# Kernel tuning notes

Measured on AMD Instinct MI355X. Metric: run time of the kernel, lower is better.

The kernel has to match this reference:

```python
import jax, jax.numpy as jnp
import numpy as np

G = 16          # horizontal stripes
K = 4           # latents per stripe
TEMP = 0.125
TOPK_RATIO = 0.125
GATE_THR = 0.05
EPS = 1e-6
KSZ = 3


def setup_inputs() -> dict:
    key = jax.random.key(0)
    k1, k2 = jax.random.split(key)
    x = jax.random.normal(k1, (64, 256, 64, 44), dtype=jnp.float32)
    latent_basis = jax.random.normal(k2, (G, K, 256), dtype=jnp.float32)
    return {"x": x, "latent_basis": latent_basis}


def _avg_pool3(x):
    # x: [n, g, c, sh, w]; 3x3 avg pool, stride 1, pad 1, count_include_pad=True
    s = jax.lax.reduce_window(x, 0.0, jax.lax.add,
                              (1, 1, 1, KSZ, KSZ), (1, 1, 1, 1, 1),
                              [(0, 0), (0, 0), (0, 0), (1, 1), (1, 1)])
    return s / float(KSZ * KSZ)


def _l2norm(v, axis=-1):
    return v / jnp.maximum(jnp.linalg.norm(v, axis=axis, keepdims=True), 1e-12)


def reference(x, latent_basis):
    n, c, h, w = x.shape
    sh = h // G
    p = sh * w
    # split into horizontal stripes: [n, g, c, sh, w]
    xr = x.reshape(n, c, G, sh, w).transpose(0, 2, 1, 3, 4)
    support_feat = _avg_pool3(xr)
    feat_flat = xr.transpose(0, 1, 3, 4, 2).reshape(n, G, p, c)          # ngpc
    support_flat = support_feat.transpose(0, 1, 3, 4, 2).reshape(n, G, p, c)

    # active mask from detached feature energy
    e = jax.lax.stop_gradient(xr).astype(jnp.float32)
    fe = jnp.mean(e * e, axis=2)                                          # n g sh w
    fe = fe / jnp.maximum(jnp.max(fe, axis=(-2, -1), keepdims=True), EPS)
    active = (fe > GATE_THR).astype(jnp.float32)
    fallback = (fe > 0).astype(jnp.float32)
    use_fb = jnp.sum(active, axis=(-2, -1), keepdims=True) <= 0
    active = jnp.where(use_fb, fallback, active).reshape(n, G, p)

    # cosine-similarity routing
    sfn = _l2norm(support_flat)
    lbn = _l2norm(latent_basis)                                           # g k c
    logits = jnp.einsum('ngpc,gkc->ngpk', sfn, lbn) / TEMP
    route_prob = jax.nn.softmax(logits, axis=-1)
    support = route_prob * active[..., None]                              # n g p k
    pool_w = support / jnp.maximum(jnp.sum(support, axis=2, keepdims=True), EPS)
    tokens = jnp.einsum('ngpk,ngpc->ngkc', pool_w, feat_flat)
    tokens = tokens.transpose(0, 3, 1, 2).reshape(n, c, G * K)            # n c (g k)

    # top-k presence
    kk = max(1, min(p, int(p * TOPK_RATIO)))
    topv, _ = jax.lax.top_k(support.transpose(0, 1, 3, 2), kk)            # n g k kk
    presence = jnp.mean(topv, axis=-1).reshape(n, G * K)
    presence = presence / jnp.maximum(jnp.sum(presence, axis=1, keepdims=True), EPS)

    # scatter per-stripe maps back into full-resolution zero tensors
    eye = jnp.eye(G, dtype=support.dtype)
    loc_s = support.reshape(n, G, sh, w, K).transpose(0, 1, 4, 2, 3)      # n g k sh w
    loc_p = pool_w.reshape(n, G, sh, w, K).transpose(0, 1, 4, 2, 3)
    smap = jnp.einsum('ngksw,gG->ngkGsw', loc_s, eye).reshape(n, G * K, h, w)
    pmap = jnp.einsum('ngksw,gG->ngkGsw', loc_p, eye).reshape(n, G * K, h, w)
    support_flat_global = smap.transpose(0, 2, 3, 1).reshape(n, h * w, G * K)
    pool_weights_flat_global = pmap.transpose(0, 2, 3, 1).reshape(n, h * w, G * K)

    return (tokens.astype(x.dtype), presence.astype(x.dtype),
            support_flat_global.astype(x.dtype), pool_weights_flat_global.astype(x.dtype))
```

## Files before the change

### kernel.cpp

```cpp
#include <hip/hip_runtime.h>
#include <math.h>

#define GG   16
#define KK   4
#define NN   64
#define CC   256
#define SHH  4
#define WW   44
#define PP   176
#define HWSZ 2816
#define CHW  720896
#define TOPKK 22

template<int CTRL, int RMASK>
__device__ __forceinline__ float dpp0(float v) {
    return __int_as_float(__builtin_amdgcn_update_dpp(
        0, __float_as_int(v), CTRL, RMASK, 0xF, true));
}

__device__ __forceinline__ float wave_sum63(float v) {
    v += dpp0<0x111, 0xF>(v);
    v += dpp0<0x112, 0xF>(v);
    v += dpp0<0x114, 0xF>(v);
    v += dpp0<0x118, 0xF>(v);
    v += dpp0<0x142, 0xA>(v);
    v += dpp0<0x143, 0xC>(v);
    return v;
}
__device__ __forceinline__ float bcast63(float v) {
    return __int_as_float(__builtin_amdgcn_readlane(__float_as_int(v), 63));
}
__device__ __forceinline__ float wave_sum_all(float v) { return bcast63(wave_sum63(v)); }

__device__ __forceinline__ float wave_max_nn(float v) {
    v = fmaxf(v, dpp0<0x111, 0xF>(v));
    v = fmaxf(v, dpp0<0x112, 0xF>(v));
    v = fmaxf(v, dpp0<0x114, 0xF>(v));
    v = fmaxf(v, dpp0<0x118, 0xF>(v));
    v = fmaxf(v, dpp0<0x142, 0xA>(v));
    v = fmaxf(v, dpp0<0x143, 0xC>(v));
    return bcast63(v);
}

__global__ __launch_bounds__(64) void norm_basis_kernel(
    const float* __restrict__ lb, float* __restrict__ lbn) {
    const int gk = blockIdx.x;
    const int lane = threadIdx.x;
    const float* row = lb + (size_t)gk * CC;
    float v0 = row[lane], v1 = row[lane + 64], v2 = row[lane + 128], v3 = row[lane + 192];
    float ss = v0 * v0 + v1 * v1 + v2 * v2 + v3 * v3;
    float tot = wave_sum_all(ss);
    float sc = 1.0f / fmaxf(sqrtf(tot), 1e-12f);
    const int g = gk >> 2, k = gk & 3;
    float* dst = lbn + (size_t)g * CC * 4 + k;
    dst[(size_t)lane * 4]        = v0 * sc;
    dst[(size_t)(lane + 64) * 4]  = v1 * sc;
    dst[(size_t)(lane + 128) * 4] = v2 * sc;
    dst[(size_t)(lane + 192) * 4] = v3 * sc;
}

__global__ __launch_bounds__(256) void stripe_kernel(
    const float* __restrict__ x, const float* __restrict__ lbn,
    float* __restrict__ sup_ws, float* __restrict__ pw_ws,
    float* __restrict__ pres_ws, float* __restrict__ tok_out) {
    const int g = blockIdx.x;
    const int n = blockIdx.y;
    const int tid = threadIdx.x;
    const int s = tid >> 6;
    const int lane = tid & 63;
    const bool al = lane < WW;

    __shared__ float4 Xq[2][SHH][WW];
    __shared__ float4 Hq[2][SHH][WW];
    __shared__ float4 sup4[PP];
    __shared__ float4 pw4[PP];
    __shared__ float redA[SHH];
    __shared__ float redB[SHH];
    __shared__ float zred[SHH][4];

    const size_t nbase = (size_t)n * CHW + (size_t)g * PP;
    const float* xrow = x + nbase + s * WW + (al ? lane : 0);
    const float4* lbg = (const float4*)lbn + (g << 8);

    float d0 = 0, d1 = 0, d2 = 0, d3 = 0, nrm = 0, fe = 0;

    int buf = 0;
    float4 xv, Hv;
    for (int c0 = 0; c0 < CC; c0 += 4, buf ^= 1) {
        if (al) {
            xv.x = xrow[(size_t)(c0 + 0) * HWSZ];
            xv.y = xrow[(size_t)(c0 + 1) * HWSZ];
            xv.z = xrow[(size_t)(c0 + 2) * HWSZ];
            xv.w = xrow[(size_t)(c0 + 3) * HWSZ];
            fe += xv.x * xv.x + xv.y * xv.y + xv.z * xv.z + xv.w * xv.w;
            Xq[buf][s][lane] = xv;
        }
        __syncthreads();
        if (al) {
            float4 L = {0, 0, 0, 0}, R = {0, 0, 0, 0};
            if (lane > 0)      L = Xq[buf][s][lane - 1];
            if (lane < WW - 1) R = Xq[buf][s][lane + 1];
            Hv.x = xv.x + L.x + R.x;
            Hv.y = xv.y + L.y + R.y;
            Hv.z = xv.z + L.z + R.z;
            Hv.w = xv.w + L.w + R.w;
            Hq[buf][s][lane] = Hv;
        }
        __syncthreads();
        if (al) {
            float4 U = {0, 0, 0, 0}, D = {0, 0, 0, 0};
            if (s > 0)       U = Hq[buf][s - 1][lane];
            if (s < SHH - 1) D = Hq[buf][s + 1][lane];
            const float k9 = 1.0f / 9.0f;
            float p0 = (Hv.x + U.x + D.x) * k9;
            float p1 = (Hv.y + U.y + D.y) * k9;
            float p2 = (Hv.z + U.z + D.z) * k9;
            float p3 = (Hv.w + U.w + D.w) * k9;
            nrm += p0 * p0 + p1 * p1 + p2 * p2 + p3 * p3;
            float4 l0 = lbg[c0], l1 = lbg[c0 + 1], l2 = lbg[c0 + 2], l3 = lbg[c0 + 3];
            d0 += p0 * l0.x + p1 * l1.x + p2 * l2.x + p3 * l3.x;
            d1 += p0 * l0.y + p1 * l1.y + p2 * l2.y + p3 * l3.y;
            d2 += p0 * l0.z + p1 * l1.z + p2 * l2.z + p3 * l3.z;
            d3 += p0 * l0.w + p1 * l1.w + p2 * l2.w + p3 * l3.w;
        }
    }

    fe *= (1.0f / 256.0f);
    float fmw = wave_max_nn(al ? fe : 0.0f);
    if (lane == 0) redA[s] = fmw;
    __syncthreads();
    float femax = fmaxf(fmaxf(redA[0], redA[1]), fmaxf(redA[2], redA[3]));
    float den = fmaxf(femax, 1e-6f);
    bool pa = al && ((fe / den) > 0.05f);
    unsigned long long bl = __ballot((int)pa);
    if (lane == 0) redB[s] = (float)__popcll(bl);
    __syncthreads();
    float cnt = redB[0] + redB[1] + redB[2] + redB[3];
    float actv = pa ? 1.0f : 0.0f;
    if (cnt <= 0.0f) actv = (al && (fe > 0.0f)) ? 1.0f : 0.0f;

    float inv = 8.0f / fmaxf(sqrtf(nrm), 1e-12f);
    float L0 = d0 * inv, L1 = d1 * inv, L2 = d2 * inv, L3 = d3 * inv;
    float mx = fmaxf(fmaxf(L0, L1), fmaxf(L2, L3));
    float e0 = expf(L0 - mx), e1 = expf(L1 - mx), e2 = expf(L2 - mx), e3 = expf(L3 - mx);
    float esum = e0 + e1 + e2 + e3;
    float sc = actv / esum;
    float s0 = e0 * sc, s1 = e1 * sc, s2 = e2 * sc, s3 = e3 * sc;

    float z0 = wave_sum63(s0), z1 = wave_sum63(s1), z2 = wave_sum63(s2), z3 = wave_sum63(s3);
    if (lane == 63) { zred[s][0] = z0; zred[s][1] = z1; zred[s][2] = z2; zred[s][3] = z3; }
    __syncthreads();
    float Z0 = zred[0][0] + zred[1][0] + zred[2][0] + zred[3][0];
    float Z1 = zred[0][1] + zred[1][1] + zred[2][1] + zred[3][1];
    float Z2 = zred[0][2] + zred[1][2] + zred[2][2] + zred[3][2];
    float Z3 = zred[0][3] + zred[1][3] + zred[2][3] + zred[3][3];
    float q0 = s0 / fmaxf(Z0, 1e-6f);
    float q1 = s1 / fmaxf(Z1, 1e-6f);
    float q2 = s2 / fmaxf(Z2, 1e-6f);
    float q3 = s3 / fmaxf(Z3, 1e-6f);

    if (al) {
        const int p = s * WW + lane;
        float4 sv = make_float4(s0, s1, s2, s3);
        float4 qv = make_float4(q0, q1, q2, q3);
        sup4[p] = sv;
        pw4[p] = qv;
        const size_t wsb = ((size_t)(n * GG + g) * PP + p);
        ((float4*)sup_ws)[wsb] = sv;
        ((float4*)pw_ws)[wsb] = qv;
    }
    __syncthreads();

    {
        const float* supf = (const float*)sup4;
        const int k = s;
        float v0 = supf[lane * 4 + k];
        float v1 = supf[(lane + 64) * 4 + k];
        float v2 = (lane < PP - 128) ? supf[(lane + 128) * 4 + k] : -1e30f;
        float tks = 0.0f;
        for (int it = 0; it < TOPKK; ++it) {
            float lm = fmaxf(v0, fmaxf(v1, v2));
            float M = wave_max_nn(lm);
            tks += M;
            unsigned long long mk = __ballot((int)(lm == M));
            int src = __ffsll(mk) - 1;
            if (lane == src) {
                if (v0 == M)      v0 = -1e30f;
                else if (v1 == M) v1 = -1e30f;
                else              v2 = -1e30f;
            }
        }
        if (lane == 0) pres_ws[(size_t)n * 64 + g * KK + k] = tks * (1.0f / (float)TOPKK);
    }

    float4 pwa = pw4[lane];
    float4 pwb = pw4[lane + 64];
    float4 pwc = (lane < PP - 128) ? pw4[lane + 128] : make_float4(0, 0, 0, 0);
    const float* xb2 = x + nbase;
    float* tokg = tok_out + (size_t)n * CC * 64 + g * KK;
    for (int i = 0; i < 64; ++i) {
        const int c = (s << 6) + i;
        const float* xc = xb2 + (size_t)c * HWSZ;
        float a0 = xc[lane];
        float a1 = xc[lane + 64];
        float a2 = (lane < PP - 128) ? xc[lane + 128] : 0.0f;
        float t0 = a0 * pwa.x + a1 * pwb.x + a2 * pwc.x;
        float t1 = a0 * pwa.y + a1 * pwb.y + a2 * pwc.y;
        float t2 = a0 * pwa.z + a1 * pwb.z + a2 * pwc.z;
        float t3 = a0 * pwa.w + a1 * pwb.w + a2 * pwc.w;
        t0 = wave_sum63(t0); t1 = wave_sum63(t1); t2 = wave_sum63(t2); t3 = wave_sum63(t3);
        if (lane == 63) {
            *(float4*)(tokg + (size_t)c * 64) = make_float4(t0, t1, t2, t3);
        }
    }
}

__global__ __launch_bounds__(256) void scatter_kernel(
    const float* __restrict__ sup_ws, const float* __restrict__ pw_ws,
    float* __restrict__ outS, float* __restrict__ outP) {
    const int t = blockIdx.x * 256 + threadIdx.x;
    const int g = t & 15;
    const int rest = t >> 4;
    const int yx = rest % HWSZ;
    const int n = rest / HWSZ;
    const int y = yx / WW;
    const int xx = yx - y * WW;
    float4 vs = make_float4(0, 0, 0, 0);
    float4 vp = make_float4(0, 0, 0, 0);
    if (g == (y >> 2)) {
        const int p = (y & 3) * WW + xx;
        const size_t base = ((size_t)(n * GG + g) * PP + p);
        vs = ((const float4*)sup_ws)[base];
        vp = ((const float4*)pw_ws)[base];
    }
    ((float4*)outS)[t] = vs;
    ((float4*)outP)[t] = vp;
}

__global__ __launch_bounds__(64) void presence_kernel(
    const float* __restrict__ pres_ws, float* __restrict__ outp) {
    const int n = blockIdx.x;
    const int lane = threadIdx.x;
    float v = pres_ws[(size_t)n * 64 + lane];
    float tot = wave_sum_all(v);
    outp[(size_t)n * 64 + lane] = v / fmaxf(tot, 1e-6f);
}

extern "C" void kernel_launch(void* const* d_in, const int* in_sizes, int n_in,
                              void* d_out, int out_size, void* d_ws, size_t ws_size,
                              hipStream_t stream) {
    const float* x = (const float*)d_in[0];
    const float* lb = (const float*)d_in[1];
    float* ws = (float*)d_ws;
    float* lbn    = ws;
    float* sup_ws = lbn + 16384;
    float* pw_ws  = sup_ws + 720896;
    float* pres_ws = pw_ws + 720896;

    float* out = (float*)d_out;
    float* tok   = out;
    float* pres  = out + 1048576;
    float* outS  = out + 1052672;
    float* outP  = outS + 11534336;

    norm_basis_kernel<<<GG * KK, 64, 0, stream>>>(lb, lbn);
    stripe_kernel<<<dim3(GG, NN), 256, 0, stream>>>(x, lbn, sup_ws, pw_ws, pres_ws, tok);
    scatter_kernel<<<(NN * HWSZ * 16) / 256, 256, 0, stream>>>(sup_ws, pw_ws, outS, outP);
    presence_kernel<<<NN, 64, 0, stream>>>(pres_ws, pres);
}
```

Before: 351.1 us.

## Split stripe kernel into channel-chunked partial, finalize and token kernels

```diff
diff --git a/kernel.cpp b/kernel.cpp
--- a/kernel.cpp
+++ b/kernel.cpp
@@ -11,6 +11,8 @@
 #define HWSZ 2816
 #define CHW  720896
 #define TOPKK 22
+#define NCHUNK 2
+#define CPC  128
 
 template<int CTRL, int RMASK>
 __device__ __forceinline__ float dpp0(float v) {
@@ -53,17 +55,17 @@
     float sc = 1.0f / fmaxf(sqrtf(tot), 1e-12f);
     const int g = gk >> 2, k = gk & 3;
     float* dst = lbn + (size_t)g * CC * 4 + k;
-    dst[(size_t)lane * 4]        = v0 * sc;
+    dst[(size_t)lane * 4]         = v0 * sc;
     dst[(size_t)(lane + 64) * 4]  = v1 * sc;
     dst[(size_t)(lane + 128) * 4] = v2 * sc;
     dst[(size_t)(lane + 192) * 4] = v3 * sc;
 }
 
-__global__ __launch_bounds__(256) void stripe_kernel(
+__global__ __launch_bounds__(256) void part_kernel(
     const float* __restrict__ x, const float* __restrict__ lbn,
-    float* __restrict__ sup_ws, float* __restrict__ pw_ws,
-    float* __restrict__ pres_ws, float* __restrict__ tok_out) {
-    const int g = blockIdx.x;
+    float4* __restrict__ dpart, float2* __restrict__ nfpart) {
+    const int g = blockIdx.x & 15;
+    const int chunk = blockIdx.x >> 4;
     const int n = blockIdx.y;
     const int tid = threadIdx.x;
     const int s = tid >> 6;
@@ -72,21 +74,17 @@
 
     __shared__ float4 Xq[2][SHH][WW];
     __shared__ float4 Hq[2][SHH][WW];
-    __shared__ float4 sup4[PP];
-    __shared__ float4 pw4[PP];
-    __shared__ float redA[SHH];
-    __shared__ float redB[SHH];
-    __shared__ float zred[SHH][4];
 
     const size_t nbase = (size_t)n * CHW + (size_t)g * PP;
     const float* xrow = x + nbase + s * WW + (al ? lane : 0);
     const float4* lbg = (const float4*)lbn + (g << 8);
+    const int cbase = chunk * CPC;
 
     float d0 = 0, d1 = 0, d2 = 0, d3 = 0, nrm = 0, fe = 0;
 
     int buf = 0;
     float4 xv, Hv;
-    for (int c0 = 0; c0 < CC; c0 += 4, buf ^= 1) {
+    for (int c0 = cbase; c0 < cbase + CPC; c0 += 4, buf ^= 1) {
         if (al) {
             xv.x = xrow[(size_t)(c0 + 0) * HWSZ];
             xv.y = xrow[(size_t)(c0 + 1) * HWSZ];
@@ -124,6 +122,40 @@
             d3 += p0 * l0.w + p1 * l1.w + p2 * l2.w + p3 * l3.w;
         }
     }
+    if (al) {
+        const size_t idx = (((size_t)(n * GG + g) * NCHUNK) + chunk) * PP + s * WW + lane;
+        dpart[idx] = make_float4(d0, d1, d2, d3);
+        nfpart[idx] = make_float2(nrm, fe);
+    }
+}
+
+__global__ __launch_bounds__(256) void finalize_kernel(
+    const float4* __restrict__ dpart, const float2* __restrict__ nfpart,
+    float* __restrict__ sup_ws, float* __restrict__ pw_ws,
+    float* __restrict__ pres_ws) {
+    const int g = blockIdx.x;
+    const int n = blockIdx.y;
+    const int tid = threadIdx.x;
+    const int s = tid >> 6;
+    const int lane = tid & 63;
+    const bool al = lane < WW;
+
+    __shared__ float4 sup4[PP];
+    __shared__ float redA[SHH];
+    __shared__ float redB[SHH];
+    __shared__ float zred[SHH][4];
+
+    float d0 = 0, d1 = 0, d2 = 0, d3 = 0, nrm = 0, fe = 0;
+    if (al) {
+        const int p = s * WW + lane;
+        const size_t b = (size_t)(n * GG + g) * NCHUNK * PP + p;
+        for (int ch = 0; ch < NCHUNK; ++ch) {
+            float4 dv = dpart[b + ch * PP];
+            float2 nf = nfpart[b + ch * PP];
+            d0 += dv.x; d1 += dv.y; d2 += dv.z; d3 += dv.w;
+            nrm += nf.x; fe += nf.y;
+        }
+    }
 
     fe *= (1.0f / 256.0f);
     float fmw = wave_max_nn(al ? fe : 0.0f);
@@ -164,7 +196,6 @@
         float4 sv = make_float4(s0, s1, s2, s3);
         float4 qv = make_float4(q0, q1, q2, q3);
         sup4[p] = sv;
-        pw4[p] = qv;
         const size_t wsb = ((size_t)(n * GG + g) * PP + p);
         ((float4*)sup_ws)[wsb] = sv;
         ((float4*)pw_ws)[wsb] = qv;
@@ -192,15 +223,29 @@
         }
         if (lane == 0) pres_ws[(size_t)n * 64 + g * KK + k] = tks * (1.0f / (float)TOPKK);
     }
-
-    float4 pwa = pw4[lane];
-    float4 pwb = pw4[lane + 64];
-    float4 pwc = (lane < PP - 128) ? pw4[lane + 128] : make_float4(0, 0, 0, 0);
-    const float* xb2 = x + nbase;
+}
+
+__global__ __launch_bounds__(256) void token_kernel(
+    const float* __restrict__ x, const float* __restrict__ pw_ws,
+    float* __restrict__ tok_out) {
+    const int g = blockIdx.x & 15;
+    const int chunk = blockIdx.x >> 4;
+    const int n = blockIdx.y;
+    const int tid = threadIdx.x;
+    const int s = tid >> 6;
+    const int lane = tid & 63;
+
+    const float4* pwq = (const float4*)pw_ws + (size_t)(n * GG + g) * PP;
+    float4 pwa = pwq[lane];
+    float4 pwb = pwq[lane + 64];
+    float4 pwc = (lane < PP - 128) ? pwq[lane + 128] : make_float4(0, 0, 0, 0);
+
+    const float* xb = x + (size_t)n * CHW + (size_t)g * PP;
     float* tokg = tok_out + (size_t)n * CC * 64 + g * KK;
-    for (int i = 0; i < 64; ++i) {
-        const int c = (s << 6) + i;
-        const float* xc = xb2 + (size_t)c * HWSZ;
+    const int cb = chunk * CPC + s * (CPC / 4);
+    for (int i = 0; i < CPC / 4; ++i) {
+        const int c = cb + i;
+        const float* xc = xb + (size_t)c * HWSZ;
         float a0 = xc[lane];
         float a1 = xc[lane + 64];
         float a2 = (lane < PP - 128) ? xc[lane + 128] : 0.0f;
@@ -216,25 +261,33 @@
 }
 
 __global__ __launch_bounds__(256) void scatter_kernel(
-    const float* __restrict__ sup_ws, const float* __restrict__ pw_ws,
-    float* __restrict__ outS, float* __restrict__ outP) {
-    const int t = blockIdx.x * 256 + threadIdx.x;
-    const int g = t & 15;
-    const int rest = t >> 4;
-    const int yx = rest % HWSZ;
-    const int n = rest / HWSZ;
-    const int y = yx / WW;
-    const int xx = yx - y * WW;
-    float4 vs = make_float4(0, 0, 0, 0);
-    float4 vp = make_float4(0, 0, 0, 0);
-    if (g == (y >> 2)) {
+    const float4* __restrict__ sup_ws4, const float4* __restrict__ pw_ws4,
+    float4* __restrict__ outS, float4* __restrict__ outP) {
+    const int n = blockIdx.y;
+    const int pix0 = blockIdx.x * 16;
+    const int t = threadIdx.x;
+    __shared__ float4 qs[16];
+    __shared__ float4 qp[16];
+    if (t < 32) {
+        const int px = t & 15;
+        const int pixel = pix0 + px;
+        const int y = pixel / WW;
+        const int xx = pixel - y * WW;
+        const int g = y >> 2;
         const int p = (y & 3) * WW + xx;
-        const size_t base = ((size_t)(n * GG + g) * PP + p);
-        vs = ((const float4*)sup_ws)[base];
-        vp = ((const float4*)pw_ws)[base];
-    }
-    ((float4*)outS)[t] = vs;
-    ((float4*)outP)[t] = vp;
+        const size_t base = (size_t)(n * GG + g) * PP + p;
+        if (t < 16) qs[px] = sup_ws4[base];
+        else        qp[px] = pw_ws4[base];
+    }
+    __syncthreads();
+    const int px = t >> 4;
+    const int q = t & 15;
+    const int pixel = pix0 + px;
+    const int g = (pixel / WW) >> 2;
+    const float4 z = make_float4(0, 0, 0, 0);
+    const size_t o = ((size_t)n * HWSZ + pixel) * 16 + q;
+    outS[o] = (q == g) ? qs[px] : z;
+    outP[o] = (q == g) ? qp[px] : z;
 }
 
 __global__ __launch_bounds__(64) void presence_kernel(
@@ -252,19 +305,26 @@
     const float* x = (const float*)d_in[0];
     const float* lb = (const float*)d_in[1];
     float* ws = (float*)d_ws;
-    float* lbn    = ws;
-    float* sup_ws = lbn + 16384;
-    float* pw_ws  = sup_ws + 720896;
+    float* lbn     = ws;
+    float* sup_ws  = lbn + 16384;
+    float* pw_ws   = sup_ws + 720896;
     float* pres_ws = pw_ws + 720896;
 
     float* out = (float*)d_out;
-    float* tok   = out;
-    float* pres  = out + 1048576;
-    float* outS  = out + 1052672;
-    float* outP  = outS + 11534336;
+    float* tok  = out;
+    float* pres = out + 1048576;
+    float* outS = out + 1052672;
+    float* outP = outS + 11534336;
+
+    float4* dpart  = (float4*)outP;
+    float2* nfpart = (float2*)(outP + 1441792 * 4 / 1);
+    nfpart = (float2*)(outP + 5767168);
 
     norm_basis_kernel<<<GG * KK, 64, 0, stream>>>(lb, lbn);
-    stripe_kernel<<<dim3(GG, NN), 256, 0, stream>>>(x, lbn, sup_ws, pw_ws, pres_ws, tok);
-    scatter_kernel<<<(NN * HWSZ * 16) / 256, 256, 0, stream>>>(sup_ws, pw_ws, outS, outP);
+    part_kernel<<<dim3(GG * NCHUNK, NN), 256, 0, stream>>>(x, lbn, dpart, nfpart);
+    finalize_kernel<<<dim3(GG, NN), 256, 0, stream>>>(dpart, nfpart, sup_ws, pw_ws, pres_ws);
+    token_kernel<<<dim3(GG * NCHUNK, NN), 256, 0, stream>>>(x, pw_ws, tok);
+    scatter_kernel<<<dim3(HWSZ / 16, NN), 256, 0, stream>>>(
+        (const float4*)sup_ws, (const float4*)pw_ws, (float4*)outS, (float4*)outP);
     presence_kernel<<<NN, 64, 0, stream>>>(pres_ws, pres);
 }
```

Result: no change. 349.1 us (-0.6%).

## Fuse scatter into stripe kernel and split channel reduction across eight waves

Applied to the files above, without the earlier changes.

```diff
diff --git a/kernel.cpp b/kernel.cpp
--- a/kernel.cpp
+++ b/kernel.cpp
@@ -17,6 +17,8 @@
     return __int_as_float(__builtin_amdgcn_update_dpp(
         0, __float_as_int(v), CTRL, RMASK, 0xF, true));
 }
+__device__ __forceinline__ float nbrL(float v) { return dpp0<0x138, 0xF>(v); }
+__device__ __forceinline__ float nbrR(float v) { return dpp0<0x130, 0xF>(v); }
 
 __device__ __forceinline__ float wave_sum63(float v) {
     v += dpp0<0x111, 0xF>(v);
@@ -53,94 +55,119 @@
     float sc = 1.0f / fmaxf(sqrtf(tot), 1e-12f);
     const int g = gk >> 2, k = gk & 3;
     float* dst = lbn + (size_t)g * CC * 4 + k;
-    dst[(size_t)lane * 4]        = v0 * sc;
+    dst[(size_t)lane * 4]         = v0 * sc;
     dst[(size_t)(lane + 64) * 4]  = v1 * sc;
     dst[(size_t)(lane + 128) * 4] = v2 * sc;
     dst[(size_t)(lane + 192) * 4] = v3 * sc;
 }
 
-__global__ __launch_bounds__(256) void stripe_kernel(
+__global__ __launch_bounds__(512, 8) void fused_kernel(
     const float* __restrict__ x, const float* __restrict__ lbn,
-    float* __restrict__ sup_ws, float* __restrict__ pw_ws,
-    float* __restrict__ pres_ws, float* __restrict__ tok_out) {
+    float* __restrict__ pres_ws, float* __restrict__ tok_out,
+    float4* __restrict__ outS, float4* __restrict__ outP) {
     const int g = blockIdx.x;
     const int n = blockIdx.y;
     const int tid = threadIdx.x;
-    const int s = tid >> 6;
+    const int w = tid >> 6;
     const int lane = tid & 63;
     const bool al = lane < WW;
 
-    __shared__ float4 Xq[2][SHH][WW];
-    __shared__ float4 Hq[2][SHH][WW];
-    __shared__ float4 sup4[PP];
-    __shared__ float4 pw4[PP];
-    __shared__ float redA[SHH];
-    __shared__ float redB[SHH];
-    __shared__ float zred[SHH][4];
-
-    const size_t nbase = (size_t)n * CHW + (size_t)g * PP;
-    const float* xrow = x + nbase + s * WW + (al ? lane : 0);
+    __shared__ float4 pd[8][PP];
+    __shared__ float2 pnf[8][PP];
+    __shared__ float redA[4], redB[4], zred[4][4];
+    float4* sup4 = pd[2];
+    float4* pw4  = pd[4];
+
+    const float* xb = x + (size_t)n * CHW + g * PP;
     const float4* lbg = (const float4*)lbn + (g << 8);
 
-    float d0 = 0, d1 = 0, d2 = 0, d3 = 0, nrm = 0, fe = 0;
-
-    int buf = 0;
-    float4 xv, Hv;
-    for (int c0 = 0; c0 < CC; c0 += 4, buf ^= 1) {
-        if (al) {
-            xv.x = xrow[(size_t)(c0 + 0) * HWSZ];
-            xv.y = xrow[(size_t)(c0 + 1) * HWSZ];
-            xv.z = xrow[(size_t)(c0 + 2) * HWSZ];
-            xv.w = xrow[(size_t)(c0 + 3) * HWSZ];
-            fe += xv.x * xv.x + xv.y * xv.y + xv.z * xv.z + xv.w * xv.w;
-            Xq[buf][s][lane] = xv;
-        }
-        __syncthreads();
-        if (al) {
-            float4 L = {0, 0, 0, 0}, R = {0, 0, 0, 0};
-            if (lane > 0)      L = Xq[buf][s][lane - 1];
-            if (lane < WW - 1) R = Xq[buf][s][lane + 1];
-            Hv.x = xv.x + L.x + R.x;
-            Hv.y = xv.y + L.y + R.y;
-            Hv.z = xv.z + L.z + R.z;
-            Hv.w = xv.w + L.w + R.w;
-            Hq[buf][s][lane] = Hv;
-        }
-        __syncthreads();
-        if (al) {
-            float4 U = {0, 0, 0, 0}, D = {0, 0, 0, 0};
-            if (s > 0)       U = Hq[buf][s - 1][lane];
-            if (s < SHH - 1) D = Hq[buf][s + 1][lane];
-            const float k9 = 1.0f / 9.0f;
-            float p0 = (Hv.x + U.x + D.x) * k9;
-            float p1 = (Hv.y + U.y + D.y) * k9;
-            float p2 = (Hv.z + U.z + D.z) * k9;
-            float p3 = (Hv.w + U.w + D.w) * k9;
-            nrm += p0 * p0 + p1 * p1 + p2 * p2 + p3 * p3;
-            float4 l0 = lbg[c0], l1 = lbg[c0 + 1], l2 = lbg[c0 + 2], l3 = lbg[c0 + 3];
-            d0 += p0 * l0.x + p1 * l1.x + p2 * l2.x + p3 * l3.x;
-            d1 += p0 * l0.y + p1 * l1.y + p2 * l2.y + p3 * l3.y;
-            d2 += p0 * l0.z + p1 * l1.z + p2 * l2.z + p3 * l3.z;
-            d3 += p0 * l0.w + p1 * l1.w + p2 * l2.w + p3 * l3.w;
-        }
-    }
-
-    fe *= (1.0f / 256.0f);
-    float fmw = wave_max_nn(al ? fe : 0.0f);
-    if (lane == 0) redA[s] = fmw;
+    float4 dk[4];
+    float nr[4] = {0, 0, 0, 0}, fe[4] = {0, 0, 0, 0};
+    #pragma unroll
+    for (int s = 0; s < 4; ++s) dk[s] = make_float4(0, 0, 0, 0);
+
+    const int c0 = w * 32;
+    float r0 = 0, r1 = 0, r2 = 0, r3 = 0;
+    if (al) {
+        const float* xc = xb + (size_t)c0 * HWSZ;
+        r0 = xc[lane]; r1 = xc[lane + 44]; r2 = xc[lane + 88]; r3 = xc[lane + 132];
+    }
+    #pragma unroll 1
+    for (int i = 0; i < 32; ++i) {
+        float b0 = 0, b1 = 0, b2 = 0, b3 = 0;
+        if (i < 31 && al) {
+            const float* xn = xb + (size_t)(c0 + i + 1) * HWSZ;
+            b0 = xn[lane]; b1 = xn[lane + 44]; b2 = xn[lane + 88]; b3 = xn[lane + 132];
+        }
+        float4 lb = lbg[c0 + i];
+        fe[0] += r0 * r0; fe[1] += r1 * r1; fe[2] += r2 * r2; fe[3] += r3 * r3;
+        float h0 = r0 + nbrL(r0) + nbrR(r0);
+        float h1 = r1 + nbrL(r1) + nbrR(r1);
+        float h2 = r2 + nbrL(r2) + nbrR(r2);
+        float h3 = r3 + nbrL(r3) + nbrR(r3);
+        const float k9 = 1.0f / 9.0f;
+        float p0 = (h0 + h1) * k9;
+        float p1 = (h0 + h1 + h2) * k9;
+        float p2 = (h1 + h2 + h3) * k9;
+        float p3 = (h2 + h3) * k9;
+        nr[0] += p0 * p0; nr[1] += p1 * p1; nr[2] += p2 * p2; nr[3] += p3 * p3;
+        dk[0].x += p0 * lb.x; dk[0].y += p0 * lb.y; dk[0].z += p0 * lb.z; dk[0].w += p0 * lb.w;
+        dk[1].x += p1 * lb.x; dk[1].y += p1 * lb.y; dk[1].z += p1 * lb.z; dk[1].w += p1 * lb.w;
+        dk[2].x += p2 * lb.x; dk[2].y += p2 * lb.y; dk[2].z += p2 * lb.z; dk[2].w += p2 * lb.w;
+        dk[3].x += p3 * lb.x; dk[3].y += p3 * lb.y; dk[3].z += p3 * lb.z; dk[3].w += p3 * lb.w;
+        r0 = b0; r1 = b1; r2 = b2; r3 = b3;
+    }
+    if (al) {
+        #pragma unroll
+        for (int s = 0; s < 4; ++s) {
+            pd[w][s * 44 + lane]  = dk[s];
+            pnf[w][s * 44 + lane] = make_float2(nr[s], fe[s]);
+        }
+    }
+    __syncthreads();
+
+    if (tid < PP) {
+        float4 a = pd[0][tid];
+        #pragma unroll
+        for (int ww = 1; ww < 8; ++ww) {
+            float4 b = pd[ww][tid];
+            a.x += b.x; a.y += b.y; a.z += b.z; a.w += b.w;
+        }
+        pd[0][tid] = a;
+    } else if (tid >= 256 && tid < 256 + PP) {
+        const int p = tid - 256;
+        float2 a = pnf[0][p];
+        #pragma unroll
+        for (int ww = 1; ww < 8; ++ww) {
+            float2 b = pnf[ww][p];
+            a.x += b.x; a.y += b.y;
+        }
+        pnf[0][p] = a;
+    }
+    __syncthreads();
+
+    const int s4 = w & 3;
+    const int pix = s4 * 44 + (al ? lane : 0);
+    float4 dv = pd[0][pix];
+    float2 nf = pnf[0][pix];
+    float nrm = nf.x;
+    float fev = nf.y * (1.0f / 256.0f);
+
+    float fmw = wave_max_nn(al ? fev : 0.0f);
+    if (w < 4 && lane == 0) redA[s4] = fmw;
     __syncthreads();
     float femax = fmaxf(fmaxf(redA[0], redA[1]), fmaxf(redA[2], redA[3]));
     float den = fmaxf(femax, 1e-6f);
-    bool pa = al && ((fe / den) > 0.05f);
+    bool pa = al && ((fev / den) > 0.05f);
     unsigned long long bl = __ballot((int)pa);
-    if (lane == 0) redB[s] = (float)__popcll(bl);
+    if (w < 4 && lane == 0) redB[s4] = (float)__popcll(bl);
     __syncthreads();
     float cnt = redB[0] + redB[1] + redB[2] + redB[3];
     float actv = pa ? 1.0f : 0.0f;
-    if (cnt <= 0.0f) actv = (al && (fe > 0.0f)) ? 1.0f : 0.0f;
+    if (cnt <= 0.0f) actv = (al && (fev > 0.0f)) ? 1.0f : 0.0f;
 
     float inv = 8.0f / fmaxf(sqrtf(nrm), 1e-12f);
-    float L0 = d0 * inv, L1 = d1 * inv, L2 = d2 * inv, L3 = d3 * inv;
+    float L0 = dv.x * inv, L1 = dv.y * inv, L2 = dv.z * inv, L3 = dv.w * inv;
     float mx = fmaxf(fmaxf(L0, L1), fmaxf(L2, L3));
     float e0 = expf(L0 - mx), e1 = expf(L1 - mx), e2 = expf(L2 - mx), e3 = expf(L3 - mx);
     float esum = e0 + e1 + e2 + e3;
@@ -148,7 +175,7 @@
     float s0 = e0 * sc, s1 = e1 * sc, s2 = e2 * sc, s3 = e3 * sc;
 
     float z0 = wave_sum63(s0), z1 = wave_sum63(s1), z2 = wave_sum63(s2), z3 = wave_sum63(s3);
-    if (lane == 63) { zred[s][0] = z0; zred[s][1] = z1; zred[s][2] = z2; zred[s][3] = z3; }
+    if (w < 4 && lane == 63) { zred[s4][0] = z0; zred[s4][1] = z1; zred[s4][2] = z2; zred[s4][3] = z3; }
     __syncthreads();
     float Z0 = zred[0][0] + zred[1][0] + zred[2][0] + zred[3][0];
     float Z1 = zred[0][1] + zred[1][1] + zred[2][1] + zred[3][1];
@@ -159,21 +186,15 @@
     float q2 = s2 / fmaxf(Z2, 1e-6f);
     float q3 = s3 / fmaxf(Z3, 1e-6f);
 
-    if (al) {
-        const int p = s * WW + lane;
-        float4 sv = make_float4(s0, s1, s2, s3);
-        float4 qv = make_float4(q0, q1, q2, q3);
-        sup4[p] = sv;
-        pw4[p] = qv;
-        const size_t wsb = ((size_t)(n * GG + g) * PP + p);
-        ((float4*)sup_ws)[wsb] = sv;
-        ((float4*)pw_ws)[wsb] = qv;
-    }
-    __syncthreads();
-
-    {
+    if (w < 4 && al) {
+        sup4[pix] = make_float4(s0, s1, s2, s3);
+        pw4[pix]  = make_float4(q0, q1, q2, q3);
+    }
+    __syncthreads();
+
+    if (w < 4) {
         const float* supf = (const float*)sup4;
-        const int k = s;
+        const int k = w;
         float v0 = supf[lane * 4 + k];
         float v1 = supf[(lane + 64) * 4 + k];
         float v2 = (lane < PP - 128) ? supf[(lane + 128) * 4 + k] : -1e30f;
@@ -193,48 +214,49 @@
         if (lane == 0) pres_ws[(size_t)n * 64 + g * KK + k] = tks * (1.0f / (float)TOPKK);
     }
 
-    float4 pwa = pw4[lane];
-    float4 pwb = pw4[lane + 64];
-    float4 pwc = (lane < PP - 128) ? pw4[lane + 128] : make_float4(0, 0, 0, 0);
-    const float* xb2 = x + nbase;
-    float* tokg = tok_out + (size_t)n * CC * 64 + g * KK;
-    for (int i = 0; i < 64; ++i) {
-        const int c = (s << 6) + i;
-        const float* xc = xb2 + (size_t)c * HWSZ;
-        float a0 = xc[lane];
-        float a1 = xc[lane + 64];
-        float a2 = (lane < PP - 128) ? xc[lane + 128] : 0.0f;
-        float t0 = a0 * pwa.x + a1 * pwb.x + a2 * pwc.x;
-        float t1 = a0 * pwa.y + a1 * pwb.y + a2 * pwc.y;
-        float t2 = a0 * pwa.z + a1 * pwb.z + a2 * pwc.z;
-        float t3 = a0 * pwa.w + a1 * pwb.w + a2 * pwc.w;
-        t0 = wave_sum63(t0); t1 = wave_sum63(t1); t2 = wave_sum63(t2); t3 = wave_sum63(t3);
-        if (lane == 63) {
-            *(float4*)(tokg + (size_t)c * 64) = make_float4(t0, t1, t2, t3);
-        }
-    }
-}
-
-__global__ __launch_bounds__(256) void scatter_kernel(
-    const float* __restrict__ sup_ws, const float* __restrict__ pw_ws,
-    float* __restrict__ outS, float* __restrict__ outP) {
-    const int t = blockIdx.x * 256 + threadIdx.x;
-    const int g = t & 15;
-    const int rest = t >> 4;
-    const int yx = rest % HWSZ;
-    const int n = rest / HWSZ;
-    const int y = yx / WW;
-    const int xx = yx - y * WW;
-    float4 vs = make_float4(0, 0, 0, 0);
-    float4 vp = make_float4(0, 0, 0, 0);
-    if (g == (y >> 2)) {
-        const int p = (y & 3) * WW + xx;
-        const size_t base = ((size_t)(n * GG + g) * PP + p);
-        vs = ((const float4*)sup_ws)[base];
-        vp = ((const float4*)pw_ws)[base];
-    }
-    ((float4*)outS)[t] = vs;
-    ((float4*)outP)[t] = vp;
+    {
+        const size_t obase = ((size_t)n * HWSZ + (size_t)g * PP) * 16;
+        const float4 z = make_float4(0, 0, 0, 0);
+        #pragma unroll 1
+        for (int j = tid; j < PP * 16; j += 512) {
+            const int px = j >> 4, q = j & 15;
+            float4 vs = sup4[px];
+            float4 vp = pw4[px];
+            bool hit = (q == g);
+            outS[obase + j] = hit ? vs : z;
+            outP[obase + j] = hit ? vp : z;
+        }
+    }
+
+    {
+        float4 pwa = pw4[lane];
+        float4 pwb = pw4[lane + 64];
+        float4 pwc = (lane < PP - 128) ? pw4[lane + 128] : make_float4(0, 0, 0, 0);
+        float* tokg = tok_out + (size_t)n * CC * 64 + g * KK;
+        const int cb = w * 32;
+        const float* xc0 = xb + (size_t)cb * HWSZ;
+        float a0 = xc0[lane];
+        float a1 = xc0[lane + 64];
+        float a2 = (lane < PP - 128) ? xc0[lane + 128] : 0.0f;
+        #pragma unroll 1
+        for (int i = 0; i < 32; ++i) {
+            float b0 = 0, b1 = 0, b2 = 0;
+            if (i < 31) {
+                const float* xn = xb + (size_t)(cb + i + 1) * HWSZ;
+                b0 = xn[lane]; b1 = xn[lane + 64];
+                b2 = (lane < PP - 128) ? xn[lane + 128] : 0.0f;
+            }
+            float t0 = a0 * pwa.x + a1 * pwb.x + a2 * pwc.x;
+            float t1 = a0 * pwa.y + a1 * pwb.y + a2 * pwc.y;
+            float t2 = a0 * pwa.z + a1 * pwb.z + a2 * pwc.z;
+            float t3 = a0 * pwa.w + a1 * pwb.w + a2 * pwc.w;
+            t0 = wave_sum63(t0); t1 = wave_sum63(t1); t2 = wave_sum63(t2); t3 = wave_sum63(t3);
+            if (lane == 63) {
+                *(float4*)(tokg + (size_t)(cb + i) * 64) = make_float4(t0, t1, t2, t3);
+            }
+            a0 = b0; a1 = b1; a2 = b2;
+        }
+    }
 }
 
 __global__ __launch_bounds__(64) void presence_kernel(
@@ -252,19 +274,17 @@
     const float* x = (const float*)d_in[0];
     const float* lb = (const float*)d_in[1];
     float* ws = (float*)d_ws;
-    float* lbn    = ws;
-    float* sup_ws = lbn + 16384;
-    float* pw_ws  = sup_ws + 720896;
-    float* pres_ws = pw_ws + 720896;
+    float* lbn     = ws;
+    float* pres_ws = lbn + 16384;
 
     float* out = (float*)d_out;
-    float* tok   = out;
-    float* pres  = out + 1048576;
-    float* outS  = out + 1052672;
-    float* outP  = outS + 11534336;
+    float* tok  = out;
+    float* pres = out + 1048576;
+    float* outS = out + 1052672;
+    float* outP = outS + 11534336;
 
     norm_basis_kernel<<<GG * KK, 64, 0, stream>>>(lb, lbn);
-    stripe_kernel<<<dim3(GG, NN), 256, 0, stream>>>(x, lbn, sup_ws, pw_ws, pres_ws, tok);
-    scatter_kernel<<<(NN * HWSZ * 16) / 256, 256, 0, stream>>>(sup_ws, pw_ws, outS, outP);
+    fused_kernel<<<dim3(GG, NN), 512, 0, stream>>>(
+        x, lbn, pres_ws, tok, (float4*)outS, (float4*)outP);
     presence_kernel<<<NN, 64, 0, stream>>>(pres_ws, pres);
 }
```

Measured after the change: 358.4 us. +2.1%, slower.
